# Kernel optimization log

Hardware: AMD Instinct MI355X
Metric: run time of the kernel (lower is better)

The kernel has to match this reference:

```python
import jax, jax.numpy as jnp
import numpy as np

NTOKEN, EMBED, HID, VDIM, MAXLEN = 15000, 1024, 1024, 2048, 20
B, NOBJ = 128, 36

def gru_cell(x, h, Wih, Whh, bih, bhh):
    gi = x @ Wih.T + bih
    gh = h @ Whh.T + bhh
    i_r, i_z, i_n = jnp.split(gi, 3, axis=-1)
    h_r, h_z, h_n = jnp.split(gh, 3, axis=-1)
    r = jax.nn.sigmoid(i_r + h_r)
    z = jax.nn.sigmoid(i_z + h_z)
    n = jnp.tanh(i_n + r * h_n)
    return (1.0 - z) * n + z * h

def setup_inputs() -> dict:
    key = jax.random.key(0)
    ks = jax.random.split(key, 20)
    s = 0.02
    inp = {
        'v': jax.random.normal(ks[0], (B, NOBJ, VDIM), jnp.float32),
        'caption': jax.random.randint(ks[1], (B, MAXLEN), 0, NTOKEN, jnp.int32),
        'cap_len': jax.random.randint(ks[2], (B,), 2, MAXLEN + 1, jnp.int32),
        'emb': jax.random.normal(ks[3], (NTOKEN, EMBED), jnp.float32) * s,
        'Wih1': jax.random.normal(ks[4], (3 * HID, HID + VDIM + EMBED), jnp.float32) * s,
        'Whh1': jax.random.normal(ks[5], (3 * HID, HID), jnp.float32) * s,
        'bih1': jnp.zeros((3 * HID,), jnp.float32),
        'bhh1': jnp.zeros((3 * HID,), jnp.float32),
        'Wih2': jax.random.normal(ks[6], (3 * HID, VDIM + HID), jnp.float32) * s,
        'Whh2': jax.random.normal(ks[7], (3 * HID, HID), jnp.float32) * s,
        'bih2': jnp.zeros((3 * HID,), jnp.float32),
        'bhh2': jnp.zeros((3 * HID,), jnp.float32),
        'Wfc1': jax.random.normal(ks[8], (HID, HID), jnp.float32) * s,
        'bfc1': jnp.zeros((HID,), jnp.float32),
        'Wfc2': jax.random.normal(ks[9], (NTOKEN, HID), jnp.float32) * s,
        'bfc2': jnp.zeros((NTOKEN,), jnp.float32),
        'Wv': jax.random.normal(ks[10], (HID, VDIM), jnp.float32) * s,
        'bv': jnp.zeros((HID,), jnp.float32),
        'Wq': jax.random.normal(ks[11], (HID, HID), jnp.float32) * s,
        'bq': jnp.zeros((HID,), jnp.float32),
        'Wa': jax.random.normal(ks[12], (1, HID), jnp.float32) * s,
        'ba': jnp.zeros((1,), jnp.float32),
    }
    return inp

def reference(v, caption, cap_len, emb, Wih1, Whh1, bih1, bhh1, Wih2, Whh2, bih2, bhh2,
              Wfc1, bfc1, Wfc2, bfc2, Wv, bv, Wq, bq, Wa, ba):
    batch, num_objs, _ = v.shape
    # sort by descending caption length (stable, matching torch sort + inverse perm)
    sort_id = jnp.argsort(-cap_len)
    restore_id = jnp.argsort(sort_id)
    cap_len_s = cap_len[sort_id]
    sort_caption = caption[sort_id]
    v_s = v[sort_id]
    v_mean = v_s.mean(axis=1)                      # [B, VDIM]
    cap_emb = emb[sort_caption]                    # [B, T, E]
    # precompute attention v-projection (relu FCNet): [B, O, HID]
    v_proj = jax.nn.relu(jnp.einsum('bod,hd->boh', v_s, Wv) + bv)
    dec_len = cap_len_s - 1
    T = cap_emb.shape[1] - 1                       # max_len - 1 decode steps
    ts = jnp.arange(T)
    mask = (ts[:, None] < dec_len[None, :])        # [T, B]
    cap_seq = jnp.swapaxes(cap_emb[:, :T, :], 0, 1)  # [T, B, E]

    def step(carry, xs):
        h1, h2 = carry
        cap_t, m_t = xs
        x1 = jnp.concatenate([h2, v_mean, cap_t], axis=1)
        h1 = gru_cell(x1, h1, Wih1, Whh1, bih1, bhh1)
        h = h1 @ Wfc1.T + bfc1
        q_proj = jax.nn.relu(h @ Wq.T + bq)        # [B, HID]
        joint = v_proj * q_proj[:, None, :]        # [B, O, HID]
        logits = jnp.einsum('boh,h->bo', joint, Wa[0]) + ba[0]
        att = jax.nn.softmax(logits, axis=1)       # [B, O]
        att_v = jnp.einsum('bo,bod->bd', att, v_s)
        h2 = gru_cell(jnp.concatenate([att_v, h], axis=1), h2, Wih2, Whh2, bih2, bhh2)
        out_t = h2 @ Wfc2.T + bfc2                 # [B, NTOKEN]
        out_t = jnp.where(m_t[:, None], out_t, 0.0)
        alpha_t = jnp.where(m_t[:, None], att, 0.0)
        return (h1, h2), (out_t, alpha_t)

    h0 = jnp.zeros((batch, HID), v.dtype)
    (_, _), (outs, alphas) = jax.lax.scan(step, (h0, h0), (cap_seq, mask))
    # pad last timestep (loop never reaches t = max_len-1) and softmax all rows
    output = jnp.concatenate([jnp.swapaxes(outs, 0, 1),
                              jnp.zeros((batch, 1, Wfc2.shape[0]), v.dtype)], axis=1)
    alpha = jnp.concatenate([jnp.swapaxes(alphas, 0, 1),
                             jnp.zeros((batch, 1, num_objs), v.dtype)], axis=1)
    predict = jax.nn.softmax(output, axis=2)[restore_id]
    return predict, sort_caption[:, 1:], alpha[restore_id]
```

## Files before the change

### kernel.cpp

```cpp
#include <hip/hip_runtime.h>
#include <math.h>

#define NTOKEN 15000
#define EMBED  1024
#define HID    1024
#define VDIM   2048
#define MAXLEN 20
#define BATCH  128
#define NOBJ   36
#define TSTEP  19

typedef unsigned short ushort_t;
typedef __attribute__((ext_vector_type(8))) short short8;
typedef __attribute__((ext_vector_type(4))) float floatx4;

__device__ __forceinline__ float b2f(ushort_t u) {
    return __uint_as_float(((unsigned)u) << 16);
}
__device__ __forceinline__ ushort_t f2b(float f) {
    unsigned x = __float_as_uint(f);
    unsigned r = (x + 0x7fffu + ((x >> 16) & 1u)) >> 16;
    return (ushort_t)r;
}

__device__ __forceinline__ void gload16(const ushort_t* g, ushort_t* l) {
    __builtin_amdgcn_global_load_lds(
        (const __attribute__((address_space(1))) unsigned int*)g,
        (__attribute__((address_space(3))) unsigned int*)l, 16, 0, 0);
}

template<int NF, bool OUT_BF16>
__device__ __forceinline__ void mfma_core(
    ushort_t* As, ushort_t* Bs,
    const ushort_t* __restrict__ A, int lda, const int* __restrict__ arow,
    const ushort_t* __restrict__ B, int ldb,
    void* __restrict__ Cv, int ldc, const int* __restrict__ crow,
    const float* __restrict__ bias, const float* __restrict__ mulvec,
    const float* __restrict__ cadd, long ldadd, int cadd_div,
    int relu_n, int N, int K, int m0, int n0, int k0)
{
    constexpr int ABUF = 128 * 32;
    constexpr int BBUF = NF * 16 * 32;
    const int tid  = threadIdx.x;
    const int lane = tid & 63;
    const int w    = tid >> 6;

    floatx4 acc[2][NF];
#pragma unroll
    for (int mf = 0; mf < 2; mf++)
#pragma unroll
        for (int nf = 0; nf < NF; nf++) acc[mf][nf] = (floatx4){0.f, 0.f, 0.f, 0.f};

    const int sr = lane >> 2;
    const int sc = lane & 3;

    int ra0 = w * 32 + sr;
    int ra1 = ra0 + 16;
    int ga0 = m0 + ra0; if (arow) ga0 = arow[ga0];
    int ga1 = m0 + ra1; if (arow) ga1 = arow[ga1];
    const ushort_t* srcA0 = A + (long)ga0 * lda + k0 + ((sc ^ (ra0 & 3)) * 8);
    const ushort_t* srcA1 = A + (long)ga1 * lda + k0 + ((sc ^ (ra1 & 3)) * 8);

    const ushort_t* srcB0;
    const ushort_t* srcB1 = nullptr;
    if constexpr (NF == 8) {
        int rb0 = w * 32 + sr, rb1 = rb0 + 16;
        int gb0 = n0 + rb0; if (gb0 >= N) gb0 = N - 1;
        int gb1 = n0 + rb1; if (gb1 >= N) gb1 = N - 1;
        srcB0 = B + (long)gb0 * ldb + k0 + ((sc ^ (rb0 & 3)) * 8);
        srcB1 = B + (long)gb1 * ldb + k0 + ((sc ^ (rb1 & 3)) * 8);
    } else {
        int rb0 = w * 16 + sr;
        int gb0 = n0 + rb0; if (gb0 >= N) gb0 = N - 1;
        srcB0 = B + (long)gb0 * ldb + k0 + ((sc ^ (rb0 & 3)) * 8);
    }

    ushort_t* Abase = As + w * 1024;
    ushort_t* Bbase = (NF == 8) ? (Bs + w * 1024) : (Bs + w * 512);

    auto STAGE = [&](int p, int kk) {
        gload16(srcA0 + kk, Abase + p * ABUF);
        gload16(srcA1 + kk, Abase + p * ABUF + 512);
        if constexpr (NF == 8) {
            gload16(srcB0 + kk, Bbase + p * BBUF);
            gload16(srcB1 + kk, Bbase + p * BBUF + 512);
        } else if constexpr (NF == 4) {
            gload16(srcB0 + kk, Bbase + p * BBUF);
        } else {
            if (w < 2) gload16(srcB0 + kk, Bbase + p * BBUF);
        }
    };

    const int fr   = lane & 15;
    const int aoff = (((lane >> 4) ^ (fr & 3)) * 8);

    auto CMP = [&](const ushort_t* Ap, const ushort_t* Bp) {
        short8 bfr[NF];
#pragma unroll
        for (int nf = 0; nf < NF; nf++)
            bfr[nf] = *(const short8*)(Bp + (nf * 16 + fr) * 32 + aoff);
#pragma unroll
        for (int mf = 0; mf < 2; mf++) {
            short8 af = *(const short8*)(Ap + (w * 32 + mf * 16 + fr) * 32 + aoff);
#pragma unroll
            for (int nf = 0; nf < NF; nf++)
                acc[mf][nf] = __builtin_amdgcn_mfma_f32_16x16x32_bf16(
                    af, bfr[nf], acc[mf][nf], 0, 0, 0);
        }
    };

    const int T = K >> 5;
    STAGE(0, 0);
    __syncthreads();
    int p = 0;
    for (int i = 0; i < T; i++) {
        if (i + 1 < T) STAGE(p ^ 1, (i + 1) * 32);
        CMP(As + p * ABUF, Bs + p * BBUF);
        __syncthreads();
        p ^= 1;
    }

    const int rq = lane >> 4;
#pragma unroll
    for (int mf = 0; mf < 2; mf++) {
#pragma unroll
        for (int r = 0; r < 4; r++) {
            int m = m0 + w * 32 + mf * 16 + rq * 4 + r;
            int cm = crow ? crow[m] : m;
            const float* caddrow = cadd ? (cadd + (long)(m / cadd_div) * ldadd) : nullptr;
#pragma unroll
            for (int nf = 0; nf < NF; nf++) {
                int n = n0 + nf * 16 + fr;
                if (n < N) {
                    float val = acc[mf][nf][r];
                    if (bias)    val += bias[n];
                    if (caddrow) val += caddrow[n];
                    if (n < relu_n) val = fmaxf(val, 0.f);
                    if (mulvec)  val *= mulvec[n];
                    if (OUT_BF16) ((ushort_t*)Cv)[(long)cm * ldc + n] = f2b(val);
                    else          ((float*)Cv)[(long)cm * ldc + n]   = val;
                }
            }
        }
    }
}

template<int NF, bool OUT_BF16>
__global__ __launch_bounds__(256) void mfma_gemm(
    const ushort_t* __restrict__ A, int lda, const int* __restrict__ arow,
    const ushort_t* __restrict__ B, int ldb,
    void* __restrict__ C, int ldc, const int* __restrict__ crow,
    const float* __restrict__ bias, const float* __restrict__ mulvec,
    const float* __restrict__ cadd, long ldadd, int cadd_div,
    int relu_n, int N, int K, int swz)
{
    __shared__ ushort_t As[2 * 128 * 32];
    __shared__ ushort_t Bs[2 * NF * 16 * 32];
    int mt = blockIdx.y, nt = blockIdx.x;
    if (swz) {
        int D = gridDim.x * gridDim.y;
        int d = blockIdx.y * gridDim.x + blockIdx.x;
        int x = d & 7, j = d >> 3, q = D >> 3, r = D & 7;
        int g = x * q + (x < r ? x : r) + j;
        mt = g % gridDim.y; nt = g / gridDim.y;
    }
    mfma_core<NF, OUT_BF16>(As, Bs, A, lda, arow, B, ldb, C, ldc, crow,
                            bias, mulvec, cadd, ldadd, cadd_div, relu_n,
                            N, K, mt * 128, nt * (NF * 16), 0);
}

template<int NF, int KS>
__global__ __launch_bounds__(256) void splitk_gemm(
    const ushort_t* __restrict__ A, int lda,
    const ushort_t* __restrict__ B, int ldb,
    float* __restrict__ C0, float* __restrict__ CP, long pstride, int ldc,
    const float* __restrict__ bias,
    const float* __restrict__ cadd, long ldadd,
    int N, int K)
{
    __shared__ ushort_t As[2 * 128 * 32];
    __shared__ ushort_t Bs[2 * NF * 16 * 32];
    const int s = blockIdx.y;
    const int Kc = K / KS;
    float* C = (s == 0) ? C0 : (CP + (long)(s - 1) * pstride);
    mfma_core<NF, false>(As, Bs, A, lda, nullptr, B, ldb, C, ldc, nullptr,
                         s == 0 ? bias : nullptr, nullptr,
                         s == 0 ? cadd : nullptr, ldadd, 1,
                         0, N, Kc, 0, blockIdx.x * (NF * 16), s * Kc);
}

template<int NF, int KS>
__global__ __launch_bounds__(256) void step3_kernel(
    const ushort_t* __restrict__ h1b, const ushort_t* __restrict__ h2b,
    const ushort_t* __restrict__ Wih1h, const ushort_t* __restrict__ Whh1b,
    const ushort_t* __restrict__ Whh2b,
    float* __restrict__ gi, float* __restrict__ gh, float* __restrict__ gh2,
    float* __restrict__ P_gi, float* __restrict__ P_gh, float* __restrict__ P_gh2,
    const float* __restrict__ gi1s_t,
    const float* __restrict__ bhh1, const float* __restrict__ bhh2)
{
    __shared__ ushort_t As[2 * 128 * 32];
    __shared__ ushort_t Bs[2 * NF * 16 * 32];
    const int s = blockIdx.y;
    const int Kc = 1024 / KS;
    const ushort_t* A; const ushort_t* B; float* C0; float* CP;
    const float* bias = nullptr; const float* cadd = nullptr;
    if (blockIdx.z == 0)      { A = h2b; B = Wih1h; C0 = gi;  CP = P_gi;  cadd = gi1s_t; }
    else if (blockIdx.z == 1) { A = h1b; B = Whh1b; C0 = gh;  CP = P_gh;  bias = bhh1; }
    else                      { A = h2b; B = Whh2b; C0 = gh2; CP = P_gh2; bias = bhh2; }
    float* C = (s == 0) ? C0 : (CP + (long)(s - 1) * 393216);
    mfma_core<NF, false>(As, Bs, A, 1024, nullptr, B, 1024, C, 3072, nullptr,
                         s == 0 ? bias : nullptr, nullptr,
                         s == 0 ? cadd : nullptr, (long)TSTEP * 3072, 1, 0,
                         3072, Kc, 0, blockIdx.x * (NF * 16), s * Kc);
}

__global__ void init_kernel(const int* __restrict__ caption,
                            int* __restrict__ tok_idx, int* __restrict__ crow20,
                            float* __restrict__ h12f, ushort_t* __restrict__ h12b)
{
    int idx = blockIdx.x * 256 + threadIdx.x;
    if (idx < BATCH * TSTEP) {
        int b = idx / TSTEP, t = idx % TSTEP;
        tok_idx[idx] = caption[b * MAXLEN + t];
        crow20[idx]  = b * MAXLEN + t;
    }
    h12f[idx] = 0.f;
    h12b[idx] = 0;
}

__global__ void sort_caption_kernel(const int* __restrict__ caption,
                                    const int* __restrict__ cap_len,
                                    float* __restrict__ out1)
{
    int i = threadIdx.x;
    if (i < BATCH) {
        int li = cap_len[i];
        int rank = 0;
        for (int j = 0; j < BATCH; j++) {
            int lj = cap_len[j];
            if (lj > li || (lj == li && j < i)) rank++;
        }
        for (int k = 0; k < TSTEP; k++)
            out1[rank * TSTEP + k] = (float)caption[i * MAXLEN + 1 + k];
    }
}

__global__ void vmean_kernel(const float* __restrict__ v,
                             float* __restrict__ vmean, ushort_t* __restrict__ vmeanb)
{
    int idx = blockIdx.x * 256 + threadIdx.x;
    int b = idx >> 11, d = idx & (VDIM - 1);
    float s = 0.f;
    for (int o = 0; o < NOBJ; o++) s += v[((long)b * NOBJ + o) * VDIM + d];
    float m = s * (1.0f / 36.0f);
    vmean[idx] = m;
    vmeanb[idx] = f2b(m);
}

__global__ void conv_kernel(const float* __restrict__ src, long ld,
                            const int* __restrict__ rowidx,
                            ushort_t* __restrict__ dst, int rows, int cols)
{
    long idx4 = ((long)blockIdx.x * 256 + threadIdx.x) * 4;
    if (idx4 >= (long)rows * cols) return;
    int r = (int)(idx4 / cols);
    int c = (int)(idx4 % cols);
    long sr = rowidx ? rowidx[r] : r;
    float4 f = *(const float4*)(src + sr * ld + c);
    dst[idx4 + 0] = f2b(f.x);
    dst[idx4 + 1] = f2b(f.y);
    dst[idx4 + 2] = f2b(f.z);
    dst[idx4 + 3] = f2b(f.w);
}

__global__ void transpose_conv_kernel(const float* __restrict__ src,
                                      ushort_t* __restrict__ dst)
{
    __shared__ float tile[32][33];
    int bx = blockIdx.x, by = blockIdx.y;
    int lx = threadIdx.x & 31, ly = threadIdx.x >> 5;
    for (int i = 0; i < 32; i += 8)
        tile[ly + i][lx] = src[(long)(by * 32 + ly + i) * 1024 + bx * 32 + lx];
    __syncthreads();
    for (int i = 0; i < 32; i += 8)
        dst[(long)(bx * 32 + ly + i) * 1024 + by * 32 + lx] = f2b(tile[lx][ly + i]);
}

__global__ void bias_fold_kernel(const float* __restrict__ Wq,
                                 const float* __restrict__ Wih2,
                                 const float* __restrict__ bfc1,
                                 const float* __restrict__ bq,
                                 const float* __restrict__ bih2,
                                 float* __restrict__ bcat2)
{
    int wave = blockIdx.x * 4 + (threadIdx.x >> 6);
    int lane = threadIdx.x & 63;
    for (int n = wave; n < 4096; n += 256) {
        const float* wrow = (n < 1024) ? (Wq + (long)n * 1024)
                                       : (Wih2 + (long)(n - 1024) * 3072 + 2048);
        float s = 0.f;
        for (int j = lane; j < 1024; j += 64) s += wrow[j] * bfc1[j];
        for (int off = 32; off > 0; off >>= 1) s += __shfl_down(s, off);
        if (lane == 0) bcat2[n] = s + ((n < 1024) ? bq[n] : bih2[n - 1024]);
    }
}

__global__ void gru_kernel(const float* __restrict__ gi, const float* __restrict__ giP,
                           const float* __restrict__ gh, const float* __restrict__ ghP,
                           int nsp,
                           float* __restrict__ h, ushort_t* __restrict__ hb,
                           ushort_t* __restrict__ hstore, int t)
{
    int idx = blockIdx.x * 256 + threadIdx.x;
    int b = idx >> 10, j = idx & (HID - 1);
    long o0 = (long)b * 3 * HID + j;
    float ir = gi[o0], iz = gi[o0 + HID], in_ = gi[o0 + 2 * HID];
    float hr = gh[o0], hz = gh[o0 + HID], hn  = gh[o0 + 2 * HID];
    for (int s = 0; s < nsp; s++) {
        const float* gp = giP + (long)s * 393216;
        const float* hp = ghP + (long)s * 393216;
        ir  += gp[o0]; iz += gp[o0 + HID]; in_ += gp[o0 + 2 * HID];
        hr  += hp[o0]; hz += hp[o0 + HID]; hn  += hp[o0 + 2 * HID];
    }
    float r = 1.f / (1.f + expf(-(ir + hr)));
    float z = 1.f / (1.f + expf(-(iz + hz)));
    float n = tanhf(in_ + r * hn);
    float hnew = (1.f - z) * n + z * h[idx];
    h[idx] = hnew;
    ushort_t hq = f2b(hnew);
    hb[idx] = hq;
    if (hstore) hstore[((long)(b * TSTEP + t) << 10) | j] = hq;
}

__global__ __launch_bounds__(512) void attn_gru2_kernel(
    const ushort_t* __restrict__ vwb, const float* __restrict__ qgi2,
    const float* __restrict__ qP,
    const ushort_t* __restrict__ vwih2,
    const float* __restrict__ gh2, const float* __restrict__ ghP2,
    const int* __restrict__ cap_len, int t,
    float* __restrict__ h2, ushort_t* __restrict__ h2b,
    ushort_t* __restrict__ hstore, float* __restrict__ alpha)
{
    int b = blockIdx.x;
    __shared__ float qs[HID];
    __shared__ float att_s[NOBJ];
    __shared__ float gis[3 * HID];
    int tid = threadIdx.x, lane = tid & 63, w = tid >> 6;
    const float* qb = qgi2 + (long)b * 4096;

    for (int hh = tid; hh < HID; hh += 512) {
        float s = qb[hh];
        for (int sp = 0; sp < 3; sp++) s += qP[(long)sp * 524288 + (long)b * 4096 + hh];
        qs[hh] = fmaxf(s, 0.f);
    }
    __syncthreads();

    for (int o = w; o < NOBJ; o += 8) {
        const ushort_t* vwo = vwb + ((long)b * NOBJ + o) * HID;
        float s = 0.f;
        for (int hh = lane * 8; hh < HID; hh += 512) {
            short8 v8 = *(const short8*)(vwo + hh);
#pragma unroll
            for (int k = 0; k < 8; k++) s += b2f((ushort_t)v8[k]) * qs[hh + k];
        }
        for (int off = 32; off > 0; off >>= 1) s += __shfl_down(s, off);
        if (lane == 0) att_s[o] = s;
    }
    __syncthreads();
    if (tid == 0) {
        float mx = att_s[0];
        for (int o = 1; o < NOBJ; o++) mx = fmaxf(mx, att_s[o]);
        float sum = 0.f;
        for (int o = 0; o < NOBJ; o++) { float e = expf(att_s[o] - mx); att_s[o] = e; sum += e; }
        float inv = 1.f / sum;
        for (int o = 0; o < NOBJ; o++) att_s[o] *= inv;
    }
    __syncthreads();
    bool m = (t < cap_len[b] - 1);
    if (tid < NOBJ) alpha[((long)b * MAXLEN + t) * NOBJ + tid] = m ? att_s[tid] : 0.f;

    const ushort_t* vw2 = vwih2 + (long)b * NOBJ * 3072;
    for (int j0 = tid * 8; j0 < 3 * HID; j0 += 512 * 8) {
        float sv[8];
        float4 qa = *(const float4*)(qb + HID + j0);
        float4 qc = *(const float4*)(qb + HID + j0 + 4);
        sv[0] = qa.x; sv[1] = qa.y; sv[2] = qa.z; sv[3] = qa.w;
        sv[4] = qc.x; sv[5] = qc.y; sv[6] = qc.z; sv[7] = qc.w;
        for (int sp = 0; sp < 3; sp++) {
            const float* qpp = qP + (long)sp * 524288 + (long)b * 4096 + HID + j0;
            float4 pa = *(const float4*)(qpp);
            float4 pc = *(const float4*)(qpp + 4);
            sv[0] += pa.x; sv[1] += pa.y; sv[2] += pa.z; sv[3] += pa.w;
            sv[4] += pc.x; sv[5] += pc.y; sv[6] += pc.z; sv[7] += pc.w;
        }
        for (int o = 0; o < NOBJ; o++) {
            float a = att_s[o];
            short8 v8 = *(const short8*)(vw2 + (long)o * 3072 + j0);
#pragma unroll
            for (int k = 0; k < 8; k++) sv[k] += a * b2f((ushort_t)v8[k]);
        }
#pragma unroll
        for (int k = 0; k < 8; k++) gis[j0 + k] = sv[k];
    }
    __syncthreads();

    for (int j = tid; j < HID; j += 512) {
        long o0 = (long)b * 3 * HID + j;
        float hr = gh2[o0], hz = gh2[o0 + HID], hn = gh2[o0 + 2 * HID];
        for (int sp = 0; sp < 3; sp++) {
            const float* hp = ghP2 + (long)sp * 393216;
            hr += hp[o0]; hz += hp[o0 + HID]; hn += hp[o0 + 2 * HID];
        }
        float ir = gis[j], iz = gis[HID + j], in_ = gis[2 * HID + j];
        float r = 1.f / (1.f + expf(-(ir + hr)));
        float z = 1.f / (1.f + expf(-(iz + hz)));
        float n = tanhf(in_ + r * hn);
        int idx = (b << 10) | j;
        float hnew = (1.f - z) * n + z * h2[idx];
        h2[idx] = hnew;
        ushort_t hq = f2b(hnew);
        h2b[idx] = hq;
        hstore[((long)(b * TSTEP + t) << 10) | j] = hq;
    }
}

__global__ __launch_bounds__(256) void softmax_kernel(float* __restrict__ predict,
                                                      float* __restrict__ alpha,
                                                      const int* __restrict__ cap_len)
{
    __shared__ float ls[NTOKEN];
    __shared__ float sred[4];
    int row = blockIdx.x;
    int b = row / MAXLEN, t = row % MAXLEN;
    float* p = predict + (long)row * NTOKEN;
    int tid = threadIdx.x;
    int dec = cap_len[b] - 1;
    if (t >= dec) {
        const float u = 1.0f / (float)NTOKEN;
        for (int i = tid; i < NTOKEN; i += 256) p[i] = u;
        if (t == MAXLEN - 1 && tid < NOBJ) alpha[(long)row * NOBJ + tid] = 0.f;
        return;
    }
    float mx = -3.4e38f;
    for (int i = tid; i < NTOKEN; i += 256) {
        float x = p[i]; ls[i] = x; mx = fmaxf(mx, x);
    }
    for (int off = 32; off > 0; off >>= 1) mx = fmaxf(mx, __shfl_down(mx, off));
    if ((tid & 63) == 0) sred[tid >> 6] = mx;
    __syncthreads();
    mx = fmaxf(fmaxf(sred[0], sred[1]), fmaxf(sred[2], sred[3]));
    __syncthreads();
    float s = 0.f;
    for (int i = tid; i < NTOKEN; i += 256) {
        float e = expf(ls[i] - mx); ls[i] = e; s += e;
    }
    for (int off = 32; off > 0; off >>= 1) s += __shfl_down(s, off);
    if ((tid & 63) == 0) sred[tid >> 6] = s;
    __syncthreads();
    s = sred[0] + sred[1] + sred[2] + sred[3];
    float inv = 1.f / s;
    for (int i = tid; i < NTOKEN; i += 256) p[i] = ls[i] * inv;
}

extern "C" void kernel_launch(void* const* d_in, const int* in_sizes, int n_in,
                              void* d_out, int out_size, void* d_ws, size_t ws_size,
                              hipStream_t stream)
{
    const float* v       = (const float*)d_in[0];
    const int*   caption = (const int*)  d_in[1];
    const int*   cap_len = (const int*)  d_in[2];
    const float* emb     = (const float*)d_in[3];
    const float* Wih1    = (const float*)d_in[4];
    const float* Whh1    = (const float*)d_in[5];
    const float* bih1    = (const float*)d_in[6];
    const float* bhh1    = (const float*)d_in[7];
    const float* Wih2    = (const float*)d_in[8];
    const float* Whh2    = (const float*)d_in[9];
    const float* bih2    = (const float*)d_in[10];
    const float* bhh2    = (const float*)d_in[11];
    const float* Wfc1    = (const float*)d_in[12];
    const float* bfc1    = (const float*)d_in[13];
    const float* Wfc2    = (const float*)d_in[14];
    const float* bfc2    = (const float*)d_in[15];
    const float* Wv      = (const float*)d_in[16];
    const float* bv      = (const float*)d_in[17];
    const float* Wq      = (const float*)d_in[18];
    const float* bq      = (const float*)d_in[19];
    const float* Wa      = (const float*)d_in[20];

    float* f32base = (float*)d_ws;
    float* gvm   = f32base;
    float* gi1s  = gvm   + 393216;
    float* h1    = gi1s  + 7471104;
    float* h2    = h1    + 131072;
    float* gi    = h2    + 131072;
    float* gh    = gi    + 393216;
    float* gh2   = gh    + 393216;
    float* qgi2  = gh2   + 393216;
    float* vmean = qgi2  + 524288;
    float* bcat2 = vmean + 262144;
    ushort_t* ub = (ushort_t*)(bcat2 + 4096);
    ushort_t* Wih1h = ub;
    ushort_t* Wih1c = Wih1h + 3145728;
    ushort_t* Whh1b = Wih1c + 3145728;
    ushort_t* Whh2b = Whh1b + 3145728;
    ushort_t* Wih2v = Whh2b + 3145728;
    ushort_t* Wcat2 = Wih2v + 6291456;
    ushort_t* Wfc2b = Wcat2 + 4194304;
    ushort_t* vw_bf = Wfc2b + 15360000;
    ushort_t* H2Ab  = vw_bf + 4718592;
    ushort_t* h1b   = H2Ab  + 2490368;
    ushort_t* h2b   = h1b   + 131072;
    ushort_t* x2v   = h2b   + 131072;
    ushort_t* vmeanb= x2v   + 262144;
    ushort_t* TEMP  = vmeanb+ 262144;
    ushort_t* vwih2 = Wfc2b;
    ushort_t* vb     = TEMP;
    ushort_t* Wvb    = TEMP + 9437184;
    ushort_t* Wqb    = TEMP;
    ushort_t* Wih2hb = TEMP + 1048576;
    ushort_t* Wfc1T  = TEMP + 4194304;
    ushort_t* Wih1m  = TEMP;
    ushort_t* Acap   = TEMP;
    float* TEMPf  = (float*)TEMP;
    float* P_gi   = TEMPf;
    float* P_gh   = P_gi  + 3 * 393216;
    float* P_gh2  = P_gh  + 3 * 393216;
    float* P_q    = P_gh2 + 3 * 393216;
    int* tok_idx = (int*)(TEMP + 11534336);
    int* crow20  = tok_idx + BATCH * TSTEP;

    float* out     = (float*)d_out;
    float* predict = out;
    float* out1    = out + (long)BATCH * MAXLEN * NTOKEN;
    float* alpha   = out1 + (long)BATCH * TSTEP;

    #define CONV(src, ld, rowidx, dst, rows, cols) \
        conv_kernel<<<(int)(((long)(rows)*(cols)/4 + 255)/256), 256, 0, stream>>>( \
            src, ld, rowidx, dst, rows, cols)

    init_kernel<<<1024, 256, 0, stream>>>(caption, tok_idx, crow20, h1, h1b);
    sort_caption_kernel<<<1, 128, 0, stream>>>(caption, cap_len, out1);
    vmean_kernel<<<(BATCH * VDIM) / 256, 256, 0, stream>>>(v, vmean, vmeanb);

    CONV(Wih1,        4096, nullptr, Wih1h, 3072, 1024);
    CONV(Wih1 + 3072, 4096, nullptr, Wih1c, 3072, 1024);
    CONV(Whh1,        1024, nullptr, Whh1b, 3072, 1024);
    CONV(Whh2,        1024, nullptr, Whh2b, 3072, 1024);
    CONV(Wih2,        3072, nullptr, Wih2v, 3072, 2048);

    CONV(v,  2048, nullptr, vb,  4608, 2048);
    CONV(Wv, 2048, nullptr, Wvb, 1024, 2048);
    mfma_gemm<8, true><<<dim3(8, 36), 256, 0, stream>>>(
        vb, 2048, nullptr, Wvb, 2048, vw_bf, 1024, nullptr,
        bv, Wa, nullptr, 0, 1, 1024, 1024, 2048, 1);

    mfma_gemm<8, true><<<dim3(24, 36), 256, 0, stream>>>(
        vb, 2048, nullptr, Wih2v, 2048, vwih2, 3072, nullptr,
        nullptr, nullptr, nullptr, 0, 1, 0, 3072, 2048, 1);

    CONV(Wq,          1024, nullptr, Wqb,    1024, 1024);
    CONV(Wih2 + 2048, 3072, nullptr, Wih2hb, 3072, 1024);
    transpose_conv_kernel<<<dim3(32, 32), 256, 0, stream>>>(Wfc1, Wfc1T);
    mfma_gemm<8, true><<<dim3(8, 8), 256, 0, stream>>>(
        Wqb, 1024, nullptr, Wfc1T, 1024, Wcat2, 1024, nullptr,
        nullptr, nullptr, nullptr, 0, 1, 0, 1024, 1024, 1);
    mfma_gemm<8, true><<<dim3(8, 24), 256, 0, stream>>>(
        Wih2hb, 1024, nullptr, Wfc1T, 1024, Wcat2 + 1048576, 1024, nullptr,
        nullptr, nullptr, nullptr, 0, 1, 0, 1024, 1024, 1);
    bias_fold_kernel<<<64, 256, 0, stream>>>(Wq, Wih2, bfc1, bq, bih2, bcat2);

    CONV(Wih1 + 1024, 4096, nullptr, Wih1m, 3072, 2048);
    mfma_gemm<8, false><<<dim3(24, 1), 256, 0, stream>>>(
        vmeanb, 2048, nullptr, Wih1m, 2048, gvm, 3072, nullptr,
        bih1, nullptr, nullptr, 0, 1, 0, 3072, 2048, 0);

    CONV(emb, 1024, tok_idx, Acap, 2432, 1024);
    mfma_gemm<8, false><<<dim3(24, 19), 256, 0, stream>>>(
        Acap, 1024, nullptr, Wih1c, 1024, gi1s, 3072, nullptr,
        nullptr, nullptr, gvm, 3072, TSTEP, 0, 3072, 1024, 1);

    for (int t = 0; t < TSTEP; t++) {
        step3_kernel<2, 4><<<dim3(96, 4, 3), 256, 0, stream>>>(
            h1b, h2b, Wih1h, Whh1b, Whh2b, gi, gh, gh2,
            P_gi, P_gh, P_gh2, gi1s + (long)t * 3072, bhh1, bhh2);
        gru_kernel<<<512, 256, 0, stream>>>(gi, P_gi, gh, P_gh, 3, h1, h1b, nullptr, t);
        splitk_gemm<2, 4><<<dim3(128, 4), 256, 0, stream>>>(
            h1b, 1024, Wcat2, 1024, qgi2, P_q, 524288, 4096,
            bcat2, nullptr, 0, 4096, 1024);
        attn_gru2_kernel<<<BATCH, 512, 0, stream>>>(
            vw_bf, qgi2, P_q, vwih2, gh2, P_gh2, cap_len, t,
            h2, h2b, H2Ab, alpha);
    }

    CONV(Wfc2, 1024, nullptr, Wfc2b, NTOKEN, 1024);
    mfma_gemm<8, false><<<dim3(118, 19), 256, 0, stream>>>(
        H2Ab, 1024, nullptr, Wfc2b, 1024, predict, NTOKEN, crow20,
        bfc2, nullptr, nullptr, 0, 1, 0, NTOKEN, 1024, 1);
    softmax_kernel<<<BATCH * MAXLEN, 256, 0, stream>>>(predict, alpha, cap_len);
    #undef CONV
}
```

Baseline: 1.934 ms.

## Compact valid output rows for final FC GEMM and split attention-GRU2 across blocks

The sort kernel now builds a compacted list of (batch, timestep) rows that are actually valid under the caption-length mask. The final vocabulary GEMM gathers only those rows through arow and crow, and exits early for 128-row tiles that are entirely padding, so the output projection work scales with real tokens. Separately, the attention+GRU2 kernel is spread over 4 blocks per batch element, each handling a 256-wide slice of the hidden dimension, for more parallelism and without the shared gate buffer. The trade-off is that the attention scores are recomputed redundantly in each of the 4 blocks, and masked rows rely on the later softmax kernel to fill them.

Result: no change. 1.925 ms (-0.5%).

```diff
diff --git a/kernel.cpp b/kernel.cpp
--- a/kernel.cpp
+++ b/kernel.cpp
@@ -131,7 +131,7 @@
 #pragma unroll
             for (int nf = 0; nf < NF; nf++) {
                 int n = n0 + nf * 16 + fr;
-                if (n < N) {
+                if (n < N && cm >= 0) {
                     float val = acc[mf][nf][r];
                     if (bias)    val += bias[n];
                     if (caddrow) val += caddrow[n];
@@ -164,6 +164,7 @@
         int g = x * q + (x < r ? x : r) + j;
         mt = g % gridDim.y; nt = g / gridDim.y;
     }
+    if (crow && crow[mt * 128] < 0) return;
     mfma_core<NF, OUT_BF16>(As, Bs, A, lda, arow, B, ldb, C, ldc, crow,
                             bias, mulvec, cadd, ldadd, cadd_div, relu_n,
                             N, K, mt * 128, nt * (NF * 16), 0);
@@ -216,14 +217,13 @@
 }
 
 __global__ void init_kernel(const int* __restrict__ caption,
-                            int* __restrict__ tok_idx, int* __restrict__ crow20,
+                            int* __restrict__ tok_idx,
                             float* __restrict__ h12f, ushort_t* __restrict__ h12b)
 {
     int idx = blockIdx.x * 256 + threadIdx.x;
     if (idx < BATCH * TSTEP) {
         int b = idx / TSTEP, t = idx % TSTEP;
         tok_idx[idx] = caption[b * MAXLEN + t];
-        crow20[idx]  = b * MAXLEN + t;
     }
     h12f[idx] = 0.f;
     h12b[idx] = 0;
@@ -231,18 +231,39 @@
 
 __global__ void sort_caption_kernel(const int* __restrict__ caption,
                                     const int* __restrict__ cap_len,
-                                    float* __restrict__ out1)
-{
+                                    float* __restrict__ out1,
+                                    int* __restrict__ arow2,
+                                    int* __restrict__ crow2)
+{
+    __shared__ int s_dec[BATCH];
+    __shared__ int ofs[BATCH + 1];
     int i = threadIdx.x;
-    if (i < BATCH) {
-        int li = cap_len[i];
-        int rank = 0;
-        for (int j = 0; j < BATCH; j++) {
-            int lj = cap_len[j];
-            if (lj > li || (lj == li && j < i)) rank++;
-        }
-        for (int k = 0; k < TSTEP; k++)
-            out1[rank * TSTEP + k] = (float)caption[i * MAXLEN + 1 + k];
+    int li = cap_len[i];
+    int dec = li - 1;
+    int rank = 0;
+    for (int j = 0; j < BATCH; j++) {
+        int lj = cap_len[j];
+        if (lj > li || (lj == li && j < i)) rank++;
+    }
+    for (int k = 0; k < TSTEP; k++)
+        out1[rank * TSTEP + k] = (float)caption[i * MAXLEN + 1 + k];
+    s_dec[i] = dec;
+    __syncthreads();
+    if (i == 0) {
+        int acc = 0;
+        for (int b = 0; b < BATCH; b++) { ofs[b] = acc; acc += s_dec[b]; }
+        ofs[BATCH] = acc;
+    }
+    __syncthreads();
+    int off = ofs[i];
+    for (int k = 0; k < dec; k++) {
+        arow2[off + k] = i * TSTEP + k;
+        crow2[off + k] = i * MAXLEN + k;
+    }
+    int total = ofs[BATCH];
+    for (int idx = total + i; idx < BATCH * TSTEP; idx += BATCH) {
+        arow2[idx] = 0;
+        crow2[idx] = -1;
     }
 }
 
@@ -333,7 +354,7 @@
     if (hstore) hstore[((long)(b * TSTEP + t) << 10) | j] = hq;
 }
 
-__global__ __launch_bounds__(512) void attn_gru2_kernel(
+__global__ __launch_bounds__(256) void attn_gru2_kernel(
     const ushort_t* __restrict__ vwb, const float* __restrict__ qgi2,
     const float* __restrict__ qP,
     const ushort_t* __restrict__ vwih2,
@@ -342,21 +363,20 @@
     float* __restrict__ h2, ushort_t* __restrict__ h2b,
     ushort_t* __restrict__ hstore, float* __restrict__ alpha)
 {
-    int b = blockIdx.x;
+    int b = blockIdx.x, y = blockIdx.y;
     __shared__ float qs[HID];
     __shared__ float att_s[NOBJ];
-    __shared__ float gis[3 * HID];
     int tid = threadIdx.x, lane = tid & 63, w = tid >> 6;
     const float* qb = qgi2 + (long)b * 4096;
 
-    for (int hh = tid; hh < HID; hh += 512) {
+    for (int hh = tid; hh < HID; hh += 256) {
         float s = qb[hh];
         for (int sp = 0; sp < 3; sp++) s += qP[(long)sp * 524288 + (long)b * 4096 + hh];
         qs[hh] = fmaxf(s, 0.f);
     }
     __syncthreads();
 
-    for (int o = w; o < NOBJ; o += 8) {
+    for (int o = w; o < NOBJ; o += 4) {
         const ushort_t* vwo = vwb + ((long)b * NOBJ + o) * HID;
         float s = 0.f;
         for (int hh = lane * 8; hh < HID; hh += 512) {
@@ -378,51 +398,39 @@
     }
     __syncthreads();
     bool m = (t < cap_len[b] - 1);
-    if (tid < NOBJ) alpha[((long)b * MAXLEN + t) * NOBJ + tid] = m ? att_s[tid] : 0.f;
-
-    const ushort_t* vw2 = vwih2 + (long)b * NOBJ * 3072;
-    for (int j0 = tid * 8; j0 < 3 * HID; j0 += 512 * 8) {
-        float sv[8];
-        float4 qa = *(const float4*)(qb + HID + j0);
-        float4 qc = *(const float4*)(qb + HID + j0 + 4);
-        sv[0] = qa.x; sv[1] = qa.y; sv[2] = qa.z; sv[3] = qa.w;
-        sv[4] = qc.x; sv[5] = qc.y; sv[6] = qc.z; sv[7] = qc.w;
-        for (int sp = 0; sp < 3; sp++) {
-            const float* qpp = qP + (long)sp * 524288 + (long)b * 4096 + HID + j0;
-            float4 pa = *(const float4*)(qpp);
-            float4 pc = *(const float4*)(qpp + 4);
-            sv[0] += pa.x; sv[1] += pa.y; sv[2] += pa.z; sv[3] += pa.w;
-            sv[4] += pc.x; sv[5] += pc.y; sv[6] += pc.z; sv[7] += pc.w;
-        }
-        for (int o = 0; o < NOBJ; o++) {
-            float a = att_s[o];
-            short8 v8 = *(const short8*)(vw2 + (long)o * 3072 + j0);
-#pragma unroll
-            for (int k = 0; k < 8; k++) sv[k] += a * b2f((ushort_t)v8[k]);
-        }
-#pragma unroll
-        for (int k = 0; k < 8; k++) gis[j0 + k] = sv[k];
-    }
-    __syncthreads();
-
-    for (int j = tid; j < HID; j += 512) {
-        long o0 = (long)b * 3 * HID + j;
-        float hr = gh2[o0], hz = gh2[o0 + HID], hn = gh2[o0 + 2 * HID];
-        for (int sp = 0; sp < 3; sp++) {
-            const float* hp = ghP2 + (long)sp * 393216;
-            hr += hp[o0]; hz += hp[o0 + HID]; hn += hp[o0 + 2 * HID];
-        }
-        float ir = gis[j], iz = gis[HID + j], in_ = gis[2 * HID + j];
-        float r = 1.f / (1.f + expf(-(ir + hr)));
-        float z = 1.f / (1.f + expf(-(iz + hz)));
-        float n = tanhf(in_ + r * hn);
-        int idx = (b << 10) | j;
-        float hnew = (1.f - z) * n + z * h2[idx];
-        h2[idx] = hnew;
-        ushort_t hq = f2b(hnew);
-        h2b[idx] = hq;
-        hstore[((long)(b * TSTEP + t) << 10) | j] = hq;
-    }
+    if (y == 0 && tid < NOBJ)
+        alpha[((long)b * MAXLEN + t) * NOBJ + tid] = m ? att_s[tid] : 0.f;
+
+    int j = y * 256 + tid;
+    long qoff = (long)b * 4096 + HID + j;
+    float ir = qgi2[qoff], iz = qgi2[qoff + 1024], in_ = qgi2[qoff + 2048];
+    for (int sp = 0; sp < 3; sp++) {
+        const float* qpp = qP + (long)sp * 524288;
+        ir += qpp[qoff]; iz += qpp[qoff + 1024]; in_ += qpp[qoff + 2048];
+    }
+    const ushort_t* vw2 = vwih2 + (long)b * NOBJ * 3072 + j;
+    for (int o = 0; o < NOBJ; o++) {
+        float a = att_s[o];
+        const ushort_t* p = vw2 + (long)o * 3072;
+        ir  += a * b2f(p[0]);
+        iz  += a * b2f(p[1024]);
+        in_ += a * b2f(p[2048]);
+    }
+    long o0 = (long)b * 3 * HID + j;
+    float hr = gh2[o0], hz = gh2[o0 + HID], hn = gh2[o0 + 2 * HID];
+    for (int sp = 0; sp < 3; sp++) {
+        const float* hp = ghP2 + (long)sp * 393216;
+        hr += hp[o0]; hz += hp[o0 + HID]; hn += hp[o0 + 2 * HID];
+    }
+    float r = 1.f / (1.f + expf(-(ir + hr)));
+    float z = 1.f / (1.f + expf(-(iz + hz)));
+    float n = tanhf(in_ + r * hn);
+    int idx = (b << 10) | j;
+    float hnew = (1.f - z) * n + z * h2[idx];
+    h2[idx] = hnew;
+    ushort_t hq = f2b(hnew);
+    h2b[idx] = hq;
+    hstore[((long)(b * TSTEP + t) << 10) | j] = hq;
 }
 
 __global__ __launch_bounds__(256) void softmax_kernel(float* __restrict__ predict,
@@ -529,7 +537,8 @@
     float* P_gh2  = P_gh  + 3 * 393216;
     float* P_q    = P_gh2 + 3 * 393216;
     int* tok_idx = (int*)(TEMP + 11534336);
-    int* crow20  = tok_idx + BATCH * TSTEP;
+    int* arow2   = tok_idx + BATCH * TSTEP;
+    int* crow2   = arow2   + BATCH * TSTEP;
 
     float* out     = (float*)d_out;
     float* predict = out;
@@ -540,8 +549,8 @@
         conv_kernel<<<(int)(((long)(rows)*(cols)/4 + 255)/256), 256, 0, stream>>>( \
             src, ld, rowidx, dst, rows, cols)
 
-    init_kernel<<<1024, 256, 0, stream>>>(caption, tok_idx, crow20, h1, h1b);
-    sort_caption_kernel<<<1, 128, 0, stream>>>(caption, cap_len, out1);
+    init_kernel<<<1024, 256, 0, stream>>>(caption, tok_idx, h1, h1b);
+    sort_caption_kernel<<<1, 128, 0, stream>>>(caption, cap_len, out1, arow2, crow2);
     vmean_kernel<<<(BATCH * VDIM) / 256, 256, 0, stream>>>(v, vmean, vmeanb);
 
     CONV(Wih1,        4096, nullptr, Wih1h, 3072, 1024);
@@ -589,14 +598,14 @@
         splitk_gemm<2, 4><<<dim3(128, 4), 256, 0, stream>>>(
             h1b, 1024, Wcat2, 1024, qgi2, P_q, 524288, 4096,
             bcat2, nullptr, 0, 4096, 1024);
-        attn_gru2_kernel<<<BATCH, 512, 0, stream>>>(
+        attn_gru2_kernel<<<dim3(BATCH, 4), 256, 0, stream>>>(
             vw_bf, qgi2, P_q, vwih2, gh2, P_gh2, cap_len, t,
             h2, h2b, H2Ab, alpha);
     }
 
     CONV(Wfc2, 1024, nullptr, Wfc2b, NTOKEN, 1024);
     mfma_gemm<8, false><<<dim3(118, 19), 256, 0, stream>>>(
-        H2Ab, 1024, nullptr, Wfc2b, 1024, predict, NTOKEN, crow20,
+        H2Ab, 1024, arow2, Wfc2b, 1024, predict, NTOKEN, crow2,
         bfc2, nullptr, nullptr, 0, 1, 0, NTOKEN, 1024, 1);
     softmax_kernel<<<BATCH * MAXLEN, 256, 0, stream>>>(predict, alpha, cap_len);
     #undef CONV
```
